# Kernel optimization log

Hardware: AMD Instinct MI355X
Metric: run time of the kernel (lower is better)

Reference implementation:

```python
import jax, jax.numpy as jnp
import numpy as np

FILTERS = 128

def setup_inputs() -> dict:
    key = jax.random.key(0)
    ks = jax.random.split(key, 8)
    B, Nq, Nkv, C = 4, 4096, 4096, 128
    q_inputs = jax.random.normal(ks[0], (B, Nq, C), dtype=jnp.float32)
    kv_inputs = jax.random.normal(ks[1], (B, Nkv, C), dtype=jnp.float32)
    s = 1.0 / np.sqrt(C)
    Wq = jax.random.normal(ks[2], (C, FILTERS), dtype=jnp.float32) * s
    Wk = jax.random.normal(ks[3], (C, FILTERS), dtype=jnp.float32) * s
    Wv = jax.random.normal(ks[4], (C, FILTERS), dtype=jnp.float32) * s
    bq = jnp.zeros((FILTERS,), jnp.float32)
    bk = jnp.zeros((FILTERS,), jnp.float32)
    bv = jnp.zeros((FILTERS,), jnp.float32)
    return {"q_inputs": q_inputs, "kv_inputs": kv_inputs,
            "Wq": Wq, "bq": bq, "Wk": Wk, "bk": bk, "Wv": Wv, "bv": bv}

def reference(q_inputs, kv_inputs, Wq, bq, Wk, bk, Wv, bv):
    # Dense projections (last-axis matmul + bias)
    q = jnp.einsum('bnc,cf->bnf', q_inputs, Wq) + bq
    k = jnp.einsum('bmc,cf->bmf', kv_inputs, Wk) + bk
    v = jnp.einsum('bmc,cf->bmf', kv_inputs, Wv) + bv
    scale = jnp.sqrt(jnp.asarray(FILTERS, jnp.float32))
    scores = jnp.einsum('bnf,bmf->bnm', q, k) / scale  # [B, Nq, Nkv]
    weights = jax.nn.softmax(scores, axis=-1)
    return jnp.einsum('bnm,bmf->bnf', weights, v)
```

## Files before the change

### kernel.cpp

```cpp
#include <hip/hip_runtime.h>
#include <stdint.h>
#include <math.h>

typedef unsigned short u16;
typedef unsigned int u32;
typedef __bf16 bf16x8 __attribute__((ext_vector_type(8)));
typedef unsigned short u16x8 __attribute__((ext_vector_type(8)));
typedef unsigned short u16x4 __attribute__((ext_vector_type(4)));
typedef float f32x4 __attribute__((ext_vector_type(4)));
typedef float f32x16 __attribute__((ext_vector_type(16)));

#define MFMA16(a, b, c) __builtin_amdgcn_mfma_f32_16x16x32_bf16((a), (b), (c), 0, 0, 0)
#define MFMA32(a, b, c) __builtin_amdgcn_mfma_f32_32x32x16_bf16((a), (b), (c), 0, 0, 0)

__device__ __forceinline__ u16 f2b(float f) {
    union { unsigned int i; float f; } v; v.f = f;
    unsigned int r = (v.i + 0x7FFFu + ((v.i >> 16) & 1u)) >> 16;
    return (u16)r;
}
__device__ __forceinline__ u32 cvtpk(float lo, float hi) {
    u32 r; asm("v_cvt_pk_bf16_f32 %0, %1, %2" : "=v"(r) : "v"(lo), "v"(hi));
    return r;
}

constexpr int N = 4096;
constexpr int Cc = 128;
constexpr int Fc = 128;
constexpr int BATCH = 4;
constexpr int NT = N / 128;

constexpr int XS_STRIDE = 136;
constexpr int WT_STRIDE = 136;
constexpr int OM_STRIDE = 130;

#define QSCALE 0.12751744750f

__global__ __launch_bounds__(256) void wtrans_kernel(
    const float* __restrict__ Wq, const float* __restrict__ Wk,
    const float* __restrict__ Wv, u16* __restrict__ WtG)
{
    __shared__ __align__(16) u16 Wl[128 * 132];
    const int tid = threadIdx.x;
    const int which = blockIdx.x;
    const float* W = which == 0 ? Wq : (which == 1 ? Wk : Wv);
#pragma unroll
    for (int it = 0; it < 16; ++it) {
        int idx4 = tid + it * 256; int e0 = idx4 * 4;
        int c = e0 >> 7, f = e0 & 127;
        float4 wv = *(const float4*)(W + e0);
        u16x4 h; h[0] = f2b(wv.x); h[1] = f2b(wv.y); h[2] = f2b(wv.z); h[3] = f2b(wv.w);
        *(u16x4*)&Wl[c * 132 + f] = h;
    }
    __syncthreads();
    u16* out = WtG + which * 16384;
#pragma unroll
    for (int it = 0; it < 8; ++it) {
        int idx8 = tid + it * 256; int e0 = idx8 * 8;
        int f = e0 >> 7, c = e0 & 127;
        u16x8 h;
#pragma unroll
        for (int j = 0; j < 8; ++j) h[j] = Wl[(c + j) * 132 + f];
        *(u16x8*)(out + e0) = h;
    }
}

__global__ __launch_bounds__(256) void proj_kernel(
    const float* __restrict__ q_in, const float* __restrict__ kv_in,
    const u16* __restrict__ WtG,
    const float* __restrict__ bq, const float* __restrict__ bk,
    const float* __restrict__ bv,
    u16* __restrict__ Qw, u16* __restrict__ Kw, u16* __restrict__ Vtw)
{
    __shared__ __align__(16) u16 Xs[64 * XS_STRIDE];
    __shared__ __align__(16) u16 Wt[128 * WT_STRIDE];

    const int tid = threadIdx.x;
    const int which = blockIdx.y;
    const int b = blockIdx.z;
    const int m0 = blockIdx.x * 64;

    const float* X = (which == 0 ? q_in : kv_in) + ((size_t)b * N + m0) * Cc;
    const u16* Wsrc = WtG + which * 16384;
    const float* bias = which == 0 ? bq : (which == 1 ? bk : bv);

#pragma unroll
    for (int it = 0; it < 8; ++it) {
        int idx4 = tid + it * 256; int e0 = idx4 * 4;
        int r = e0 >> 7, c = e0 & 127;
        float4 xv = *(const float4*)(X + e0);
        u16x4 h; h[0] = f2b(xv.x); h[1] = f2b(xv.y); h[2] = f2b(xv.z); h[3] = f2b(xv.w);
        *(u16x4*)&Xs[r * XS_STRIDE + c] = h;
    }
#pragma unroll
    for (int it = 0; it < 8; ++it) {
        int idx8 = tid + it * 256; int e0 = idx8 * 8;
        int f = e0 >> 7, c = e0 & 127;
        *(u16x8*)&Wt[f * WT_STRIDE + c] = *(const u16x8*)(Wsrc + e0);
    }
    __syncthreads();

    const int lane = tid & 63;
    const int w = tid >> 6;
    const int n16 = lane & 15;
    const int quad = lane >> 4;

    if (which < 2) {
        bf16x8 ax[4];
#pragma unroll
        for (int kk = 0; kk < 4; ++kk)
            ax[kk] = *(const bf16x8*)&Xs[(w * 16 + n16) * XS_STRIDE + kk * 32 + quad * 8];
        const float scale = (which == 0) ? QSCALE : 1.0f;
#pragma unroll
        for (int ft = 0; ft < 8; ++ft) {
            f32x4 acc = {0.f, 0.f, 0.f, 0.f};
#pragma unroll
            for (int kk = 0; kk < 4; ++kk) {
                bf16x8 bw = *(const bf16x8*)&Wt[(ft * 16 + n16) * WT_STRIDE + kk * 32 + quad * 8];
                acc = MFMA16(ax[kk], bw, acc);
            }
            float bias_f = bias[ft * 16 + n16];
#pragma unroll
            for (int r = 0; r < 4; ++r) {
                int row = m0 + w * 16 + quad * 4 + r;
                int f = ft * 16 + n16;
                u16 val = f2b((acc[r] + bias_f) * scale);
                if (which == 0) {
                    Qw[((size_t)b * N + row) * Fc + f] = val;
                } else {
                    int kgrp = row >> 5, l31r = row & 31;
                    int kk2 = f >> 4, hig = (f >> 3) & 1, jj = f & 7;
                    Kw[((size_t)b * 1024 + kgrp * 8 + kk2) * 512
                       + (hig * 32 + l31r) * 8 + jj] = val;
                }
            }
        }
    } else {
#pragma unroll
        for (int ft2 = 0; ft2 < 2; ++ft2) {
            int ftg = w * 2 + ft2;
            bf16x8 aw[4];
#pragma unroll
            for (int kk = 0; kk < 4; ++kk)
                aw[kk] = *(const bf16x8*)&Wt[(ftg * 16 + n16) * WT_STRIDE + kk * 32 + quad * 8];
            float bias4[4];
#pragma unroll
            for (int r = 0; r < 4; ++r) bias4[r] = bias[ftg * 16 + quad * 4 + r];
#pragma unroll
            for (int nt = 0; nt < 4; ++nt) {
                f32x4 acc = {0.f, 0.f, 0.f, 0.f};
#pragma unroll
                for (int kk = 0; kk < 4; ++kk) {
                    bf16x8 bx = *(const bf16x8*)&Xs[(nt * 16 + n16) * XS_STRIDE + kk * 32 + quad * 8];
                    acc = MFMA16(aw[kk], bx, acc);
                }
#pragma unroll
                for (int r = 0; r < 4; ++r) {
                    int fg = ftg * 16 + quad * 4 + r;
                    int rowg = m0 + nt * 16 + n16;
                    int kgrp = rowg >> 5, ks = (rowg >> 4) & 1;
                    int hig = (rowg >> 3) & 1, jj = rowg & 7;
                    int cb = fg >> 5, l31r = fg & 31;
                    Vtw[((size_t)b * 1024 + kgrp * 8 + cb * 2 + ks) * 512
                        + (hig * 32 + l31r) * 8 + jj] = f2b(acc[r] + bias4[r]);
                }
            }
        }
    }
}

__global__ __launch_bounds__(512, 2) void attn_kernel(
    const u16* __restrict__ Qw, const u16* __restrict__ Kw,
    const u16* __restrict__ Vtw, float* __restrict__ out)
{
    __shared__ __align__(16) char smem[134144];

    const int tid = threadIdx.x;
    const int id = blockIdx.x + 64 * blockIdx.y;
    const int b = (id >> 1) & 3;
    const int q0 = (((id & 1) << 5) + (id >> 3)) << 6;

    const int lane = tid & 63;
    const int w = tid >> 6;
    const int kg = w & 3;
    const int qg = w >> 2;
    const int l31 = lane & 31;
    const int hi = lane >> 5;

    bf16x8 aq[8];
    {
        const u16* qp = Qw + ((size_t)b * N + q0 + qg * 32 + l31) * Cc + hi * 8;
#pragma unroll
        for (int kk = 0; kk < 8; ++kk) aq[kk] = *(const bf16x8*)(qp + kk * 16);
    }

    const u16* const kfb = Kw + ((size_t)b * 1024 + kg * 8) * 512 + lane * 8;
    const u16* const vfb = Vtw + ((size_t)b * 1024 + kg * 8) * 512 + lane * 8;

    f32x16 o[4];
#pragma unroll
    for (int cb = 0; cb < 4; ++cb)
#pragma unroll
        for (int i = 0; i < 16; ++i) o[cb][i] = 0.f;
    float lloc = 0.f;

    bf16x8 kf0[8], kf1[8], vf[8];

    auto LOADK = [&](bf16x8* kf, int t) {
        const u16* p = kfb + (size_t)t * 16384;
#pragma unroll
        for (int kk = 0; kk < 8; ++kk)
            kf[kk] = *(const bf16x8*)(p + kk * 512);
    };
    auto LOADV = [&](int t) {
        const u16* p = vfb + (size_t)t * 16384;
#pragma unroll
        for (int g = 0; g < 8; ++g)
            vf[g] = *(const bf16x8*)(p + g * 512);
    };

    auto COMPUTE = [&](const bf16x8* kf) {
        f32x16 st;
#pragma unroll
        for (int i = 0; i < 16; ++i) st[i] = 0.f;
        __builtin_amdgcn_s_setprio(1);
#pragma unroll
        for (int kk = 0; kk < 8; ++kk)
            st = MFMA32(kf[kk], aq[kk], st);
        __builtin_amdgcn_s_setprio(0);
        float p[16];
#pragma unroll
        for (int i = 0; i < 16; ++i) p[i] = exp2f(st[i]);
        lloc += ((((p[0] + p[1]) + (p[2] + p[3])) + ((p[4] + p[5]) + (p[6] + p[7])))
               + (((p[8] + p[9]) + (p[10] + p[11])) + ((p[12] + p[13]) + (p[14] + p[15]))));
        bf16x8 pb[2];
#pragma unroll
        for (int ks = 0; ks < 2; ++ks) {
            u32 a0 = cvtpk(p[ks * 8 + 0], p[ks * 8 + 1]);
            u32 a1 = cvtpk(p[ks * 8 + 2], p[ks * 8 + 3]);
            u32 a2 = cvtpk(p[ks * 8 + 4], p[ks * 8 + 5]);
            u32 a3 = cvtpk(p[ks * 8 + 6], p[ks * 8 + 7]);
            auto s02 = __builtin_amdgcn_permlane32_swap(a0, a2, false, false);
            auto s13 = __builtin_amdgcn_permlane32_swap(a1, a3, false, false);
            union { u32 u[4]; bf16x8 v; } bb;
            bb.u[0] = s02[0]; bb.u[1] = s13[0]; bb.u[2] = s02[1]; bb.u[3] = s13[1];
            pb[ks] = bb.v;
        }
        __builtin_amdgcn_s_setprio(1);
#pragma unroll
        for (int cb = 0; cb < 4; ++cb) {
            o[cb] = MFMA32(vf[cb * 2 + 0], pb[0], o[cb]);
            o[cb] = MFMA32(vf[cb * 2 + 1], pb[1], o[cb]);
        }
        __builtin_amdgcn_s_setprio(0);
    };

    LOADK(kf0, 0);
    for (int t = 0; t < NT; t += 2) {
        LOADV(t);
        if (t + 1 < NT) LOADK(kf1, t + 1);
        COMPUTE(kf0);
        if (t + 1 < NT) {
            LOADV(t + 1);
            if (t + 2 < NT) LOADK(kf0, t + 2);
            COMPUTE(kf1);
        }
    }

    float lv = lloc + __shfl_xor(lloc, 32);

    float* const Om = (float*)smem;
    float* const Lm = (float*)(smem + 4 * 64 * OM_STRIDE * 4);

    const int qrow_w = qg * 32 + l31;
    const int crow0 = 4 * hi;
    {
        float* dst = Om + (size_t)(kg * 64 + qrow_w) * OM_STRIDE;
#pragma unroll
        for (int cb = 0; cb < 4; ++cb)
#pragma unroll
            for (int i = 0; i < 16; ++i) {
                int ch = cb * 32 + (i & 3) + 8 * (i >> 2) + crow0;
                dst[ch] = o[cb][i];
            }
        if (hi == 0) Lm[kg * 64 + qrow_w] = lv;
    }
    __syncthreads();

    const int qrow = tid >> 3;
    const int ch0 = (tid & 7) * 16;
    const float lsum = Lm[qrow] + Lm[64 + qrow] + Lm[128 + qrow] + Lm[192 + qrow];
    const float linv = 1.0f / lsum;
    float* op = out + ((size_t)b * N + q0 + qrow) * Fc + ch0;
#pragma unroll
    for (int j4 = 0; j4 < 4; ++j4) {
        f32x4 v;
#pragma unroll
        for (int jj = 0; jj < 4; ++jj) {
            int ch = ch0 + j4 * 4 + jj;
            float s = Om[(size_t)(0 * 64 + qrow) * OM_STRIDE + ch]
                    + Om[(size_t)(1 * 64 + qrow) * OM_STRIDE + ch]
                    + Om[(size_t)(2 * 64 + qrow) * OM_STRIDE + ch]
                    + Om[(size_t)(3 * 64 + qrow) * OM_STRIDE + ch];
            v[jj] = s * linv;
        }
        *(f32x4*)(op + j4 * 4) = v;
    }
}

extern "C" void kernel_launch(void* const* d_in, const int* in_sizes, int n_in,
                              void* d_out, int out_size, void* d_ws, size_t ws_size,
                              hipStream_t stream) {
    (void)in_sizes; (void)n_in; (void)out_size; (void)ws_size;
    const float* q_in  = (const float*)d_in[0];
    const float* kv_in = (const float*)d_in[1];
    const float* Wq = (const float*)d_in[2];
    const float* bq = (const float*)d_in[3];
    const float* Wk = (const float*)d_in[4];
    const float* bk = (const float*)d_in[5];
    const float* Wv = (const float*)d_in[6];
    const float* bv = (const float*)d_in[7];

    const size_t qkv = (size_t)BATCH * N * Fc;
    u16* Qw  = (u16*)d_ws;
    u16* Kw  = Qw + qkv;
    u16* Vtw = Kw + qkv;
    u16* WtG = Vtw + qkv;

    wtrans_kernel<<<dim3(3), dim3(256), 0, stream>>>(Wq, Wk, Wv, WtG);
    proj_kernel<<<dim3(64, 3, BATCH), dim3(256), 0, stream>>>(
        q_in, kv_in, WtG, bq, bk, bv, Qw, Kw, Vtw);
    attn_kernel<<<dim3(64, BATCH), dim3(512), 0, stream>>>(
        Qw, Kw, Vtw, (float*)d_out);
}
```

Before: 135.6 us.

## Double-buffer V fragments and split QK MFMA chain into two accumulators

Adds a second V register buffer so V for the next tile loads during the current tile's compute, and K for tile t+2 is prefetched right after the QK MFMAs. The QK dot product is split into two independent accumulator chains summed afterwards, which shortens the MFMA dependency chain. This raises register pressure (an extra 8 bf16x8 V buffer plus a second accumulator), which could reduce occupancy or cause spills. The loop now assumes NT is even, since the second STEP runs unconditionally.

```diff
diff --git a/kernel.cpp b/kernel.cpp
--- a/kernel.cpp
+++ b/kernel.cpp
@@ -203,7 +203,7 @@
         for (int i = 0; i < 16; ++i) o[cb][i] = 0.f;
     float lloc = 0.f;
 
-    bf16x8 kf0[8], kf1[8], vf[8];
+    bf16x8 kf0[8], kf1[8], vf0[8], vf1[8];
 
     auto LOADK = [&](bf16x8* kf, int t) {
         const u16* p = kfb + (size_t)t * 16384;
@@ -211,22 +211,28 @@
         for (int kk = 0; kk < 8; ++kk)
             kf[kk] = *(const bf16x8*)(p + kk * 512);
     };
-    auto LOADV = [&](int t) {
+    auto LOADV = [&](bf16x8* vf, int t) {
         const u16* p = vfb + (size_t)t * 16384;
 #pragma unroll
         for (int g = 0; g < 8; ++g)
             vf[g] = *(const bf16x8*)(p + g * 512);
     };
 
-    auto COMPUTE = [&](const bf16x8* kf) {
-        f32x16 st;
-#pragma unroll
-        for (int i = 0; i < 16; ++i) st[i] = 0.f;
+    auto STEP = [&](const bf16x8* kfc, const bf16x8* vfc,
+                    bf16x8* kfn, int tk, bf16x8* vfn, int tv) {
+        if (tv < NT) LOADV(vfn, tv);
+        f32x16 sa, sb;
+#pragma unroll
+        for (int i = 0; i < 16; ++i) { sa[i] = 0.f; sb[i] = 0.f; }
         __builtin_amdgcn_s_setprio(1);
 #pragma unroll
-        for (int kk = 0; kk < 8; ++kk)
-            st = MFMA32(kf[kk], aq[kk], st);
+        for (int kk = 0; kk < 4; ++kk) {
+            sa = MFMA32(kfc[2 * kk + 0], aq[2 * kk + 0], sa);
+            sb = MFMA32(kfc[2 * kk + 1], aq[2 * kk + 1], sb);
+        }
         __builtin_amdgcn_s_setprio(0);
+        if (tk < NT) LOADK(kfn, tk);
+        f32x16 st = sa + sb;
         float p[16];
 #pragma unroll
         for (int i = 0; i < 16; ++i) p[i] = exp2f(st[i]);
@@ -248,22 +254,18 @@
         __builtin_amdgcn_s_setprio(1);
 #pragma unroll
         for (int cb = 0; cb < 4; ++cb) {
-            o[cb] = MFMA32(vf[cb * 2 + 0], pb[0], o[cb]);
-            o[cb] = MFMA32(vf[cb * 2 + 1], pb[1], o[cb]);
+            o[cb] = MFMA32(vfc[cb * 2 + 0], pb[0], o[cb]);
+            o[cb] = MFMA32(vfc[cb * 2 + 1], pb[1], o[cb]);
         }
         __builtin_amdgcn_s_setprio(0);
     };
 
     LOADK(kf0, 0);
+    LOADV(vf0, 0);
+    LOADK(kf1, 1);
     for (int t = 0; t < NT; t += 2) {
-        LOADV(t);
-        if (t + 1 < NT) LOADK(kf1, t + 1);
-        COMPUTE(kf0);
-        if (t + 1 < NT) {
-            LOADV(t + 1);
-            if (t + 2 < NT) LOADK(kf0, t + 2);
-            COMPUTE(kf1);
-        }
+        STEP(kf0, vf0, kf0, t + 2, vf1, t + 1);
+        STEP(kf1, vf1, kf1, t + 3, vf0, t + 2);
     }
 
     float lv = lloc + __shfl_xor(lloc, 32);
```

New measurement: 192.9 us. 42.3% more time.

## Stage V tiles through LDS with async global_load_lds double buffering

Applied to the files above, without the earlier changes.

V tiles are no longer loaded by each wave directly into registers. The whole block now copies each V tile into a double-buffered LDS region using global_load_lds, and the PV MFMAs read their operands from LDS. This aims to free VGPRs, cut redundant global traffic across the wave groups that share a V tile, and overlap the V fetch with compute. In exchange it adds two block-wide barriers per tile pair and LDS read latency inside the MFMA loop.

```diff
diff --git a/kernel.cpp b/kernel.cpp
--- a/kernel.cpp
+++ b/kernel.cpp
@@ -21,6 +21,11 @@
 __device__ __forceinline__ u32 cvtpk(float lo, float hi) {
     u32 r; asm("v_cvt_pk_bf16_f32 %0, %1, %2" : "=v"(r) : "v"(lo), "v"(hi));
     return r;
+}
+__device__ __forceinline__ void gload16(const void* g, void* l) {
+    __builtin_amdgcn_global_load_lds(
+        (const __attribute__((address_space(1))) u32*)g,
+        (__attribute__((address_space(3))) u32*)l, 16, 0, 0);
 }
 
 constexpr int N = 4096;
@@ -173,6 +178,8 @@
     const u16* __restrict__ Vtw, float* __restrict__ out)
 {
     __shared__ __align__(16) char smem[134144];
+    u16* const Vs0 = (u16*)smem;
+    u16* const Vs1 = (u16*)(smem + 32768);
 
     const int tid = threadIdx.x;
     const int id = blockIdx.x + 64 * blockIdx.y;
@@ -194,7 +201,8 @@
     }
 
     const u16* const kfb = Kw + ((size_t)b * 1024 + kg * 8) * 512 + lane * 8;
-    const u16* const vfb = Vtw + ((size_t)b * 1024 + kg * 8) * 512 + lane * 8;
+    const u16* const Vtile = Vtw + (size_t)b * 1024 * 512;
+    const int vro = kg * 4096 + lane * 8;
 
     f32x16 o[4];
 #pragma unroll
@@ -203,22 +211,26 @@
         for (int i = 0; i < 16; ++i) o[cb][i] = 0.f;
     float lloc = 0.f;
 
-    bf16x8 kf0[8], kf1[8], vf[8];
-
+    bf16x8 kf0[8], kf1[8];
+
+    int ci[4];
+#pragma unroll
+    for (int it = 0; it < 4; ++it) ci[it] = tid + it * 512;
+
+    auto STAGE_V = [&](u16* vd, int t) {
+        const u16* src = Vtile + (size_t)t * 16384;
+#pragma unroll
+        for (int it = 0; it < 4; ++it)
+            gload16(src + ci[it] * 8, vd + ci[it] * 8);
+    };
     auto LOADK = [&](bf16x8* kf, int t) {
         const u16* p = kfb + (size_t)t * 16384;
 #pragma unroll
         for (int kk = 0; kk < 8; ++kk)
             kf[kk] = *(const bf16x8*)(p + kk * 512);
     };
-    auto LOADV = [&](int t) {
-        const u16* p = vfb + (size_t)t * 16384;
-#pragma unroll
-        for (int g = 0; g < 8; ++g)
-            vf[g] = *(const bf16x8*)(p + g * 512);
-    };
-
-    auto COMPUTE = [&](const bf16x8* kf) {
+
+    auto COMPUTE = [&](const bf16x8* kf, const u16* Vsb) {
         f32x16 st;
 #pragma unroll
         for (int i = 0; i < 16; ++i) st[i] = 0.f;
@@ -248,22 +260,25 @@
         __builtin_amdgcn_s_setprio(1);
 #pragma unroll
         for (int cb = 0; cb < 4; ++cb) {
-            o[cb] = MFMA32(vf[cb * 2 + 0], pb[0], o[cb]);
-            o[cb] = MFMA32(vf[cb * 2 + 1], pb[1], o[cb]);
+            bf16x8 av0 = *(const bf16x8*)(Vsb + vro + (cb * 2 + 0) * 512);
+            bf16x8 av1 = *(const bf16x8*)(Vsb + vro + (cb * 2 + 1) * 512);
+            o[cb] = MFMA32(av0, pb[0], o[cb]);
+            o[cb] = MFMA32(av1, pb[1], o[cb]);
         }
         __builtin_amdgcn_s_setprio(0);
     };
 
+    STAGE_V(Vs0, 0);
     LOADK(kf0, 0);
+    __syncthreads();
     for (int t = 0; t < NT; t += 2) {
-        LOADV(t);
-        if (t + 1 < NT) LOADK(kf1, t + 1);
-        COMPUTE(kf0);
-        if (t + 1 < NT) {
-            LOADV(t + 1);
-            if (t + 2 < NT) LOADK(kf0, t + 2);
-            COMPUTE(kf1);
-        }
+        STAGE_V(Vs1, t + 1);
+        LOADK(kf1, t + 1);
+        COMPUTE(kf0, Vs0);
+        __syncthreads();
+        if (t + 2 < NT) { STAGE_V(Vs0, t + 2); LOADK(kf0, t + 2); }
+        COMPUTE(kf1, Vs1);
+        __syncthreads();
     }
 
     float lv = lloc + __shfl_xor(lloc, 32);
```

Result: no change. 137.9 us (+1.8%).
